# Kernel tuning notes

Hardware: AMD Instinct MI355X
Metric: run time of the kernel (lower is better)

Reference implementation:

```python
import jax, jax.numpy as jnp
import numpy as np

N_GRAPHS = 256
GRADES = jnp.array([0, 1, 1, 1, 2, 2, 2, 3])      # blade -> grade for Cl(3,0): [1,e1,e2,e3,e12,e13,e23,e123]
G_ONEHOT = jnp.eye(4)[GRADES]                      # (8,4) blade->grade one-hot
NUM_RBF, CUTOFF, NEG_SLOPE = 20, 10.0, 0.2
HID, HEADS, HD, LAYERS = 64, 4, 16, 4
EPS_LN = 1e-6


def _mv_linear_sub(x, w, b):
    # MVLinear with per-grade weights. x:(N,I,8), w:(4,O,I), b:(O,) added to scalar blade.
    wb = w[GRADES]                                 # (8,O,I)
    out = jnp.einsum('nib,boi->nob', x, wb)
    return out.at[..., 0].add(b)


def _gat_layer(h, src, dst, edge_scalar, pw, pb, asrc, adst, wsrc, wdst):
    N = h.shape[0]
    z = _mv_linear_sub(h, pw, pb).reshape(N, HEADS, HD, 8)
    # fold per-grade importance weights into per-blade contraction vectors
    a_s = asrc * wsrc[:, GRADES][:, None, :]       # (H,C,8)
    a_d = adst * wdst[:, GRADES][:, None, :]
    s_src = jnp.einsum('nhcb,hcb->nh', z, a_s)
    s_dst = jnp.einsum('nhcb,hcb->nh', z, a_d)
    e = jax.nn.leaky_relu(s_src[src] + s_dst[dst] + edge_scalar, NEG_SLOPE)  # (E,H)
    e_max = jax.ops.segment_max(e, dst, num_segments=N)
    alpha = jnp.exp(e - e_max[dst])
    a_sum = jax.ops.segment_sum(alpha, dst, num_segments=N)
    alpha = alpha / (a_sum[dst] + 1e-16)
    out = jax.ops.segment_sum(z[src] * alpha[:, :, None, None], dst, num_segments=N)
    return out.reshape(N, HEADS * HD, 8)


def _mv_silu(x, a, b):
    # x:(N,C,8); a,b:(C,4). Gate by scalar part (grade 0) and per-grade squared magnitudes.
    qg = jnp.einsum('ncb,bg->ncg', x * x, G_ONEHOT)                 # (N,C,4) mag2 per grade
    norms = jnp.concatenate([x[..., :1], qg[..., 1:]], axis=-1)     # (N,C,4)
    gate = jax.nn.sigmoid(a * norms + b)[..., GRADES]               # (N,C,8)
    return gate * x


def _mv_layernorm(x, a):
    n = jnp.sqrt(jnp.sum(x * x, axis=-1))                           # (N,C)
    n = jnp.mean(n, axis=1, keepdims=True) + EPS_LN                 # (N,1)
    return a[None, :, None] * x / n[..., None]


def _forward(floats, z, edge_index, batch):
    (pos, atom_w, inw, inb, ew1, eb1, ew2, eb2,
     proj_w, proj_b, a_src, a_dst, w_src, w_dst,
     ln_a, silu_a, silu_b, ppw, ppb, pw1, pb1, pw2, pb2) = floats
    src, dst = edge_index[0], edge_index[1]
    N = pos.shape[0]

    # RBF edge features -> per-head scalar bias
    d2 = jnp.sum((pos[src] - pos[dst]) ** 2, axis=-1)
    dist = jnp.where(d2 > 0, jnp.sqrt(jnp.where(d2 > 0, d2, 1.0)), 0.0)
    centers = jnp.linspace(0.0, CUTOFF, NUM_RBF)
    width = CUTOFF / (NUM_RBF - 1)
    rbf = jnp.exp(-0.5 * ((dist[:, None] - centers) / width) ** 2)  # (E,20)
    edge_scalar = jax.nn.silu(rbf @ ew1.T + eb1) @ ew2.T + eb2      # (E,H)

    # node multivector embedding: scalars from atom embedding, grade-1 from centered positions
    h_sca = jnp.zeros((N, HID, 8), dtype=pos.dtype).at[..., 0].set(atom_w[z])
    cnt = jax.ops.segment_sum(jnp.ones((N,), pos.dtype), batch, num_segments=N_GRAPHS)
    pos_mean = jax.ops.segment_sum(pos, batch, num_segments=N_GRAPHS) / jnp.maximum(cnt, 1.0)[:, None]
    pos_c = pos - pos_mean[batch]
    h_vec = jnp.zeros((N, 1, 8), dtype=pos.dtype).at[:, 0, 1:4].set(pos_c)
    h = jnp.concatenate([h_sca, h_vec], axis=1)                     # (N,HID+1,8)
    h = jnp.einsum('nib,oi->nob', h, inw).at[..., 0].add(inb)       # input_proj, subspaces=False

    for l in range(LAYERS):
        h_res = h
        h = _gat_layer(h, src, dst, edge_scalar, proj_w[l], proj_b[l],
                       a_src[l], a_dst[l], w_src[l], w_dst[l])
        h = _mv_silu(h, silu_a[l], silu_b[l])
        h = h + h_res
        h = _mv_layernorm(h, ln_a[l])

    h = _mv_linear_sub(h, ppw, ppb)[..., 0]                         # (N,HID) scalar blade
    g = jax.ops.segment_sum(h, batch, num_segments=N_GRAPHS)        # 'add' readout -> (B,HID)
    out = jax.nn.silu(g @ pw1.T + pb1) @ pw2.T + pb2                # (B,1)
    return out[:, 0]


def setup_inputs() -> dict:
    key = jax.random.key(0)
    ks = jax.random.split(key, 24)
    N, E, B = 20000, 320000, N_GRAPHS
    rn = lambda k, shape, s=0.1: jax.random.normal(k, shape, jnp.float32) * s
    return dict(
        pos=jax.random.normal(ks[0], (N, 3), jnp.float32) * 3.0,
        z=jax.random.randint(ks[1], (N,), 0, 100),
        edge_index=jax.random.randint(ks[2], (2, E), 0, N),
        batch=jnp.sort(jax.random.randint(ks[3], (N,), 0, B)),
        atom_embed_w=rn(ks[4], (100, HID)),
        inproj_w=rn(ks[5], (HID, HID + 1)),
        inproj_b=rn(ks[6], (HID,)),
        edge_w1=rn(ks[7], (HID, NUM_RBF)),
        edge_b1=rn(ks[8], (HID,)),
        edge_w2=rn(ks[9], (HEADS, HID)),
        edge_b2=rn(ks[10], (HEADS,)),
        proj_w=rn(ks[11], (LAYERS, 4, HID, HID)),
        proj_b=rn(ks[12], (LAYERS, HID)),
        a_src=rn(ks[13], (LAYERS, HEADS, HD, 8)),
        a_dst=rn(ks[14], (LAYERS, HEADS, HD, 8)),
        w_src=jnp.ones((LAYERS, HEADS, 4), jnp.float32),
        w_dst=jnp.ones((LAYERS, HEADS, 4), jnp.float32),
        ln_a=jnp.ones((LAYERS, HID), jnp.float32),
        silu_a=jnp.ones((LAYERS, HID, 4), jnp.float32),
        silu_b=jnp.zeros((LAYERS, HID, 4), jnp.float32),
        prepool_w=rn(ks[15], (4, HID, HID)),
        prepool_b=rn(ks[16], (HID,)),
        post_w1=rn(ks[17], (HID, HID)),
        post_b1=rn(ks[18], (HID,)),
        post_w2=rn(ks[19], (1, HID)),
        post_b2=rn(ks[20], (1,)),
    )


def reference(pos, z, edge_index, batch, atom_embed_w, inproj_w, inproj_b,
              edge_w1, edge_b1, edge_w2, edge_b2, proj_w, proj_b,
              a_src, a_dst, w_src, w_dst, ln_a, silu_a, silu_b,
              prepool_w, prepool_b, post_w1, post_b1, post_w2, post_b2):
    floats = (pos, atom_embed_w, inproj_w, inproj_b, edge_w1, edge_b1, edge_w2, edge_b2,
              proj_w, proj_b, a_src, a_dst, w_src, w_dst,
              ln_a, silu_a, silu_b, prepool_w, prepool_b, post_w1, post_b1, post_w2, post_b2)
    return _forward(floats, z, edge_index, batch)
```

## Files before the change

### kernel.cpp

```cpp
#include <hip/hip_runtime.h>
#include <hip/hip_bf16.h>
#include <math.h>

#define HID 64
#define HEADS 4
#define LAYERS 4
#define NRBF 20
#define NG 256
#define CB 512
#define HSTRIDE 68
#define CAPB 64
#define TABN 8192
#define NATOM 100

typedef __attribute__((ext_vector_type(8))) short short8;
typedef __attribute__((ext_vector_type(4))) float floatx4;

__device__ __forceinline__ int gradeOf(int b){ return (b==0)?0:((b<4)?1:((b<7)?2:3)); }
__device__ __forceinline__ unsigned short f2bf(float f){
    __hip_bfloat16 h = __float2bfloat16(f);
    return *(unsigned short*)&h;
}
__device__ __forceinline__ float bflo(int u){ return __uint_as_float(((unsigned)u)<<16); }
__device__ __forceinline__ float bfhi(int u){ return __uint_as_float(((unsigned)u)&0xFFFF0000u); }
__device__ __forceinline__ int packbf2(float a, float b){
    return (int)f2bf(a) | ((int)f2bf(b)<<16);
}

struct P {
    const float *pos; const int *zidx; const int *ei; const int *batch;
    const float *atom_w, *inproj_w, *inproj_b, *ew1, *eb1, *ew2, *eb2;
    const float *proj_w, *proj_b, *a_src, *a_dst, *w_src, *w_dst;
    const float *ln_a, *silu_a, *silu_b, *ppw, *ppb, *pw1, *pb1, *pw2, *pb2;
    float *out;
    int *counts; float *possum; float *pcnt; float *gbuf;
    int *bucket;
    int *escb;
    float *tab;
    unsigned short *WTbf; float *ppw0T; float *w1T; float *sbf;
    float *embT;
    unsigned short *hb;
    unsigned short *zA; unsigned short *zB;
    float *ssA; float *sdA; float *ssB; float *sdB;
    int N, E, Mtiles;
};

__global__ __launch_bounds__(256) void k1_kernel(P p){
    const int PREP_TOTAL = LAYERS*4*64*64 + 2*HID*HID + 2*LAYERS*HEADS;
    const int CP = (PREP_TOTAL+255)/256;
    const int CG = NG/4;
    const int CT = (TABN+1+3)/4;
    int bid = blockIdx.x, t = threadIdx.x;
    if (bid < CP){
        int idx = bid*256 + t;
        const int szW = LAYERS*4*64*64;
        const int e2 = szW + HID*HID;
        const int e3 = e2 + HID*HID;
        if (idx < szW){
            p.WTbf[idx] = f2bf(p.proj_w[idx]);
        } else if (idx < e2){
            int r = idx - szW; int i = r/HID, o = r%HID;
            p.ppw0T[r] = p.ppw[o*HID + i];
        } else if (idx < e3){
            int r = idx - e2; int i = r/HID, o = r%HID;
            p.w1T[r] = p.pw1[o*HID + i];
        } else if (idx < e3 + 2*LAYERS*HEADS){
            int r = idx - e3;
            int hh = r & 3; int type = (r>>2)&1; int l = r>>3;
            const float* a = type ? p.a_dst : p.a_src;
            const float* w = type ? p.w_dst : p.w_src;
            float wh = w[l*16 + hh*4 + 0];
            float s = 0.f;
            for (int c=0;c<16;c++)
                s += a[l*512 + (hh*16+c)*8 + 0] * wh * p.proj_b[l*64 + hh*16 + c];
            p.sbf[r] = s;
        }
    } else if (bid < CP+CG){
        int wv = t>>6, lane = t&63;
        int g = (bid-CP)*4 + wv;
        int lo = 0, hi = p.N;
        while (lo < hi){ int mid = (lo+hi)>>1; if (p.batch[mid] < g) lo = mid+1; else hi = mid; }
        int s0 = lo;
        hi = p.N;
        while (lo < hi){ int mid = (lo+hi)>>1; if (p.batch[mid] < g+1) lo = mid+1; else hi = mid; }
        int s1 = lo;
        float sx=0.f, sy=0.f, sz=0.f;
        for (int i=s0+lane; i<s1; i+=64){
            sx += p.pos[i*3+0]; sy += p.pos[i*3+1]; sz += p.pos[i*3+2];
        }
        #pragma unroll
        for (int off=1; off<64; off<<=1){
            sx += __shfl_xor(sx,off,64);
            sy += __shfl_xor(sy,off,64);
            sz += __shfl_xor(sz,off,64);
        }
        if (lane==0){
            p.possum[g*3+0]=sx; p.possum[g*3+1]=sy; p.possum[g*3+2]=sz;
            p.pcnt[g] = (float)(s1-s0);
        }
    } else if (bid < CP+CG+CT){
        int wv = t>>6, lane = t&63;
        int i = (bid-CP-CG)*4 + wv;
        if (i > TABN) return;
        float d = (float)i * (16.0f/TABN);
        float t0 = d * (19.0f/10.0f);
        float hv = p.eb1[lane];
        #pragma unroll
        for (int k=0;k<NRBF;k++){
            float a = t0 - (float)k;
            hv += __expf(-0.5f*a*a) * p.ew1[lane*NRBF+k];
        }
        float act = hv/(1.0f+__expf(-hv));
        float p0 = act*p.ew2[0*HID+lane];
        float p1 = act*p.ew2[1*HID+lane];
        float p2 = act*p.ew2[2*HID+lane];
        float p3 = act*p.ew2[3*HID+lane];
        #pragma unroll
        for (int off=1; off<64; off<<=1){
            p0 += __shfl_xor(p0,off,64);
            p1 += __shfl_xor(p1,off,64);
            p2 += __shfl_xor(p2,off,64);
            p3 += __shfl_xor(p3,off,64);
        }
        if (lane==0){
            *(float4*)&p.tab[(size_t)i*4] = make_float4(p0+p.eb2[0], p1+p.eb2[1],
                                                        p2+p.eb2[2], p3+p.eb2[3]);
        }
    } else {
        int wv = t>>6, lane = t&63;
        int za = (bid-CP-CG-CT)*4 + wv;
        if (za >= NATOM) return;
        float accv = p.inproj_b[lane];
        for (int i=0;i<HID;i++)
            accv += p.atom_w[(size_t)za*HID + i] * p.inproj_w[lane*65 + i];
        p.embT[(size_t)za*HID + lane] = accv;
    }
}

__device__ __forceinline__ void proj_core(const P& p, int pl, int n0, int nt, int lane,
        const unsigned short* hAl,
        unsigned short* zout, float* ssout, float* sdout){
    const unsigned short* WTl = p.WTbf + (size_t)pl*4*64*64;
    const float* pbl = p.proj_b + pl*HID;
    const float* a_src_l = p.a_src + pl*512;
    const float* a_dst_l = p.a_dst + pl*512;
    const float* w_src_l = p.w_src + pl*16;
    const float* w_dst_l = p.w_dst + pl*16;
    const float* sb_l = p.sbf + pl*8;
    int m = lane&15, quad = lane>>4;
    int o = nt*16 + m;
    float cs[4][2][4];
    float pss[4], psd[4];
    #pragma unroll
    for (int r=0;r<4;r++){ pss[r]=0.f; psd[r]=0.f; }
    #pragma unroll
    for (int bp=0; bp<4; bp++){
        const int b0 = 2*bp, b1 = b0+1;
        const int g0 = gradeOf(b0), g1 = gradeOf(b1);
        const short8 a0 = *(const short8*)(hAl + (b0*16+m)*HSTRIDE + quad*8);
        const short8 a1 = *(const short8*)(hAl + (b0*16+m)*HSTRIDE + 32 + quad*8);
        const short8 a2 = *(const short8*)(hAl + (b1*16+m)*HSTRIDE + quad*8);
        const short8 a3 = *(const short8*)(hAl + (b1*16+m)*HSTRIDE + 32 + quad*8);
        const short8 w00 = *(const short8*)(WTl + (g0*64 + o)*64 + quad*8);
        const short8 w01 = *(const short8*)(WTl + (g0*64 + o)*64 + 32 + quad*8);
        short8 w10, w11;
        if (g1==g0){ w10 = w00; w11 = w01; }
        else {
            w10 = *(const short8*)(WTl + (g1*64 + o)*64 + quad*8);
            w11 = *(const short8*)(WTl + (g1*64 + o)*64 + 32 + quad*8);
        }
        floatx4 c0 = {0.f,0.f,0.f,0.f}, c1 = {0.f,0.f,0.f,0.f};
        c0 = __builtin_amdgcn_mfma_f32_16x16x32_bf16(a0, w00, c0, 0,0,0);
        c0 = __builtin_amdgcn_mfma_f32_16x16x32_bf16(a1, w01, c0, 0,0,0);
        c1 = __builtin_amdgcn_mfma_f32_16x16x32_bf16(a2, w10, c1, 0,0,0);
        c1 = __builtin_amdgcn_mfma_f32_16x16x32_bf16(a3, w11, c1, 0,0,0);
        float as0 = a_src_l[o*8+b0]*w_src_l[nt*4+g0];
        float as1 = a_src_l[o*8+b1]*w_src_l[nt*4+g1];
        float ad0 = a_dst_l[o*8+b0]*w_dst_l[nt*4+g0];
        float ad1 = a_dst_l[o*8+b1]*w_dst_l[nt*4+g1];
        float bias0 = (bp==0) ? pbl[o] : 0.0f;
        #pragma unroll
        for (int r=0;r<4;r++){
            float v0 = c0[r], v1 = c1[r];
            pss[r] += v0*as0 + v1*as1;
            psd[r] += v0*ad0 + v1*ad1;
            cs[bp][0][r] = v0 + bias0;
            cs[bp][1][r] = v1;
        }
    }
    #pragma unroll
    for (int r=0;r<4;r++){
        int nn = n0 + quad*4 + r;
        if (nn < p.N){
            unsigned short pk[8];
            #pragma unroll
            for (int bp=0;bp<4;bp++){
                pk[2*bp]   = f2bf(cs[bp][0][r]);
                pk[2*bp+1] = f2bf(cs[bp][1][r]);
            }
            *(int4*)(zout + (size_t)nn*CB + o*8) = *(int4*)pk;
        }
    }
    #pragma unroll
    for (int r=0;r<4;r++){
        float vs = pss[r], vd = psd[r];
        #pragma unroll
        for (int off=1; off<16; off<<=1){
            vs += __shfl_xor(vs, off, 64);
            vd += __shfl_xor(vd, off, 64);
        }
        int nn = n0 + quad*4 + r;
        if (m==0 && nn<p.N){
            ssout[nn*4+nt] = vs + sb_l[nt];
            sdout[nn*4+nt] = vd + sb_l[4+nt];
        }
    }
}

__global__ __launch_bounds__(256) void k2_kernel(P p){
    __shared__ unsigned short hAl[8*16*HSTRIDE];
    int t = threadIdx.x, wv = t>>6, lane = t&63;
    if ((int)blockIdx.x >= p.Mtiles){
        int e = ((int)blockIdx.x - p.Mtiles)*256 + t;
        if (e >= p.E) return;
        int s = p.ei[e], d = p.ei[p.E+e];
        float dx = p.pos[s*3+0]-p.pos[d*3+0];
        float dy = p.pos[s*3+1]-p.pos[d*3+1];
        float dz = p.pos[s*3+2]-p.pos[d*3+2];
        float dist = sqrtf(dx*dx+dy*dy+dz*dz);
        float idxf = fminf(dist * ((float)TABN/16.0f), (float)(TABN-1));
        int i0 = (int)idxf;
        float fr = idxf - (float)i0;
        float4 f0 = *(const float4*)&p.tab[(size_t)i0*4];
        float4 f1 = *(const float4*)&p.tab[(size_t)(i0+1)*4];
        int slot = atomicAdd(&p.counts[d],1);
        if (slot < CAPB){
            p.bucket[(size_t)d*CAPB + slot] = s;
            int2 epk = make_int2(
                packbf2(f0.x + (f1.x-f0.x)*fr, f0.y + (f1.y-f0.y)*fr),
                packbf2(f0.z + (f1.z-f0.z)*fr, f0.w + (f1.w-f0.w)*fr));
            *(int2*)&p.escb[((size_t)d*CAPB + slot)*2] = epk;
        }
        return;
    }
    int n0 = blockIdx.x*16;
    float wvv = p.inproj_w[lane*65 + 64];
    for (int k=0;k<4;k++){
        int m = wv*4 + k;
        int n = n0 + m;
        if (n < p.N){
            int zn = p.zidx[n];
            float acc = p.embT[(size_t)zn*HID + lane];
            int g = p.batch[n];
            float cm = p.pcnt[g]; cm = cm>1.0f?cm:1.0f;
            float px = p.pos[n*3+0]-p.possum[g*3+0]/cm;
            float py = p.pos[n*3+1]-p.possum[g*3+1]/cm;
            float pz = p.pos[n*3+2]-p.possum[g*3+2]/cm;
            unsigned short pk[8];
            pk[0]=f2bf(acc); pk[1]=f2bf(wvv*px); pk[2]=f2bf(wvv*py); pk[3]=f2bf(wvv*pz);
            pk[4]=0; pk[5]=0; pk[6]=0; pk[7]=0;
            *(int4*)(p.hb + (size_t)n*CB + lane*8) = *(int4*)pk;
            #pragma unroll
            for (int b=0;b<8;b++) hAl[(b*16+m)*HSTRIDE + lane] = pk[b];
        } else {
            #pragma unroll
            for (int b=0;b<8;b++) hAl[(b*16+m)*HSTRIDE + lane] = 0;
        }
    }
    __syncthreads();
    proj_core(p, 0, n0, wv, lane, hAl, p.zA, p.ssA, p.sdA);
}

__device__ __forceinline__ void fmab8(const float* lwv, int h_id, int J,
                                      const int4* zv, float* acc, float& dn){
    #pragma unroll
    for (int i=0;i<8;i++){
        float w = lwv[(J+i)*4 + h_id];
        acc[0] += w*bflo(zv[i].x); acc[1] += w*bfhi(zv[i].x);
        acc[2] += w*bflo(zv[i].y); acc[3] += w*bfhi(zv[i].y);
        acc[4] += w*bflo(zv[i].z); acc[5] += w*bfhi(zv[i].z);
        acc[6] += w*bflo(zv[i].w); acc[7] += w*bfhi(zv[i].w);
        dn += w;
    }
}

__device__ __forceinline__ void agg_node(const P& p, int l, int n, int lane, float* lwv,
        const unsigned short* __restrict__ zin, const float* __restrict__ ssin,
        const float* __restrict__ sdin, float* outv){
    int4 hres = *((const int4*)(p.hb + (size_t)n*CB) + lane);
    float4 sdl = *(const float4*)&sdin[n*4];
    int deg = min(p.counts[n], CAPB);
    int h_id = lane>>4;
    const int* bs = p.bucket + (size_t)n*CAPB;
    int s = 0;
    float l0=-1e30f,l1=-1e30f,l2=-1e30f,l3=-1e30f;
    if (lane < deg){
        s = bs[lane];
        int2 ev = *((const int2*)p.escb + ((size_t)n*CAPB + lane));
        float4 sv  = *(const float4*)&ssin[s*4];
        l0 = sv.x+sdl.x+bflo(ev.x); l0=(l0>=0.f)?l0:0.2f*l0;
        l1 = sv.y+sdl.y+bfhi(ev.x); l1=(l1>=0.f)?l1:0.2f*l1;
        l2 = sv.z+sdl.z+bflo(ev.y); l2=(l2>=0.f)?l2:0.2f*l2;
        l3 = sv.w+sdl.w+bfhi(ev.y); l3=(l3>=0.f)?l3:0.2f*l3;
    }
    int bc = (deg+7)>>3;
    int4 zv[8];
    if (bc>0){
        #pragma unroll
        for (int i=0;i<8;i++){
            int sb = __builtin_amdgcn_readlane(s, i);
            zv[i] = *((const int4*)(zin + (size_t)(unsigned)sb*CB) + lane);
        }
    }
    float m0=l0,m1=l1,m2=l2,m3=l3;
    #pragma unroll
    for (int off=1; off<64; off<<=1){
        m0=fmaxf(m0,__shfl_xor(m0,off,64));
        m1=fmaxf(m1,__shfl_xor(m1,off,64));
        m2=fmaxf(m2,__shfl_xor(m2,off,64));
        m3=fmaxf(m3,__shfl_xor(m3,off,64));
    }
    *(float4*)&lwv[lane*4] = make_float4(__expf(l0-m0),__expf(l1-m1),
                                         __expf(l2-m2),__expf(l3-m3));
    float acc[8];
    #pragma unroll
    for (int k=0;k<8;k++) acc[k]=0.f;
    float dn = 0.f;
    if (bc>0) fmab8(lwv, h_id, 0, zv, acc, dn);
    for (int j=8; j<bc*8; j+=8){
        #pragma unroll
        for (int i=0;i<8;i++){
            int sb = __builtin_amdgcn_readlane(s, j+i);
            zv[i] = *((const int4*)(zin + (size_t)(unsigned)sb*CB) + lane);
        }
        fmab8(lwv, h_id, j, zv, acc, dn);
    }
    float inv = 1.0f/(dn + 1e-16f);
    float x[8];
    #pragma unroll
    for (int k=0;k<8;k++) x[k] = acc[k]*inv;
    const float* silu_a_l = p.silu_a + l*HID*4;
    const float* silu_b_l = p.silu_b + l*HID*4;
    float4 sa = *(const float4*)&silu_a_l[lane*4];
    float4 sb = *(const float4*)&silu_b_l[lane*4];
    float n1 = x[1]*x[1]+x[2]*x[2]+x[3]*x[3];
    float n2 = x[4]*x[4]+x[5]*x[5]+x[6]*x[6];
    float n3 = x[7]*x[7];
    float g0 = 1.0f/(1.0f+__expf(-(sa.x*x[0]+sb.x)));
    float g1 = 1.0f/(1.0f+__expf(-(sa.y*n1+sb.y)));
    float g2 = 1.0f/(1.0f+__expf(-(sa.z*n2+sb.z)));
    float g3 = 1.0f/(1.0f+__expf(-(sa.w*n3+sb.w)));
    float val[8];
    val[0]=g0*x[0]+bflo(hres.x); val[1]=g1*x[1]+bfhi(hres.x);
    val[2]=g1*x[2]+bflo(hres.y); val[3]=g1*x[3]+bfhi(hres.y);
    val[4]=g2*x[4]+bflo(hres.z); val[5]=g2*x[5]+bfhi(hres.z);
    val[6]=g2*x[6]+bflo(hres.w); val[7]=g3*x[7]+bfhi(hres.w);
    float ssq=0.f;
    #pragma unroll
    for (int k=0;k<8;k++) ssq += val[k]*val[k];
    float nr = sqrtf(ssq);
    #pragma unroll
    for (int off=1; off<64; off<<=1) nr += __shfl_xor(nr, off, 64);
    float mean = nr*(1.0f/64.0f) + 1e-6f;
    float scale = p.ln_a[l*HID + lane]/mean;
    #pragma unroll
    for (int k=0;k<8;k++) outv[k] = scale*val[k];
}

__global__ __launch_bounds__(1024) void aggproj_kernel(P p, int l,
        const unsigned short* __restrict__ zin, const float* __restrict__ ssin,
        const float* __restrict__ sdin,
        unsigned short* zout, float* ssout, float* sdout){
    __shared__ float lw[16][256];
    __shared__ unsigned short hAl[8*16*HSTRIDE];
    int wv = threadIdx.x>>6, lane = threadIdx.x&63;
    int n0 = blockIdx.x*16;
    int n = n0 + wv;
    unsigned short pk[8] = {0,0,0,0,0,0,0,0};
    if (n < p.N){
        float outv[8];
        agg_node(p, l, n, lane, lw[wv], zin, ssin, sdin, outv);
        #pragma unroll
        for (int k=0;k<8;k++) pk[k] = f2bf(outv[k]);
        *(int4*)(p.hb + (size_t)n*CB + lane*8) = *(int4*)pk;
    }
    #pragma unroll
    for (int b=0;b<8;b++) hAl[(b*16+wv)*HSTRIDE + lane] = pk[b];
    __syncthreads();
    if (wv < 4)
        proj_core(p, l+1, n0, wv, lane, hAl, zout, ssout, sdout);
}

__global__ __launch_bounds__(256) void agg_kernel(P p, int l,
        const unsigned short* __restrict__ zin, const float* __restrict__ ssin,
        const float* __restrict__ sdin){
    __shared__ float lw[4][256];
    int wv = threadIdx.x>>6, lane = threadIdx.x&63;
    int n = blockIdx.x*4 + wv;
    if (n >= p.N) return;
    float outv[8];
    agg_node(p, l, n, lane, lw[wv], zin, ssin, sdin, outv);
    atomicAdd(&p.gbuf[p.batch[n]*HID + lane], outv[0]);
}

__global__ void final_kernel(P p){
    int gid = blockIdx.x; int o = threadIdx.x;
    float gs = p.gbuf[gid*HID + o];
    float cnt = p.pcnt[gid];
    float gsc = cnt * p.ppb[o];
    for (int i=0;i<HID;i++) gsc += __shfl(gs, i, 64) * p.ppw0T[i*HID + o];
    float a = p.pb1[o];
    for (int i=0;i<HID;i++) a += __shfl(gsc, i, 64) * p.w1T[i*HID + o];
    float act = a/(1.0f+__expf(-a));
    float pv = act * p.pw2[o];
    #pragma unroll
    for (int off=1; off<64; off<<=1) pv += __shfl_xor(pv, off, 64);
    if (o==0) p.out[gid] = pv + p.pb2[0];
}

extern "C" void kernel_launch(void* const* d_in, const int* in_sizes, int n_in,
                              void* d_out, int out_size, void* d_ws, size_t ws_size,
                              hipStream_t stream) {
    P p;
    p.pos      = (const float*)d_in[0];
    p.zidx     = (const int*)  d_in[1];
    p.ei       = (const int*)  d_in[2];
    p.batch    = (const int*)  d_in[3];
    p.atom_w   = (const float*)d_in[4];
    p.inproj_w = (const float*)d_in[5];
    p.inproj_b = (const float*)d_in[6];
    p.ew1      = (const float*)d_in[7];
    p.eb1      = (const float*)d_in[8];
    p.ew2      = (const float*)d_in[9];
    p.eb2      = (const float*)d_in[10];
    p.proj_w   = (const float*)d_in[11];
    p.proj_b   = (const float*)d_in[12];
    p.a_src    = (const float*)d_in[13];
    p.a_dst    = (const float*)d_in[14];
    p.w_src    = (const float*)d_in[15];
    p.w_dst    = (const float*)d_in[16];
    p.ln_a     = (const float*)d_in[17];
    p.silu_a   = (const float*)d_in[18];
    p.silu_b   = (const float*)d_in[19];
    p.ppw      = (const float*)d_in[20];
    p.ppb      = (const float*)d_in[21];
    p.pw1      = (const float*)d_in[22];
    p.pb1      = (const float*)d_in[23];
    p.pw2      = (const float*)d_in[24];
    p.pb2      = (const float*)d_in[25];
    p.out = (float*)d_out;

    const int N = in_sizes[0]/3;
    const int E = in_sizes[2]/2;
    p.N = N; p.E = E; p.Mtiles = (N+15)/16;

    float* wsf = (float*)d_ws;
    size_t off = 0;
    auto alloc = [&](size_t nelem){ size_t r = off; off += (nelem + 63) & ~(size_t)63; return r; };
    size_t o_counts = alloc(N);
    size_t o_g      = alloc(NG*HID);
    size_t zero_end = off;
    size_t o_possum = alloc(NG*3);
    size_t o_pcnt   = alloc(NG);
    size_t o_bucket = alloc((size_t)N*CAPB);
    size_t o_escb   = alloc((size_t)N*CAPB*2);
    size_t o_tab    = alloc((size_t)(TABN+2)*4);
    size_t o_ssA    = alloc((size_t)N*4);
    size_t o_sdA    = alloc((size_t)N*4);
    size_t o_ssB    = alloc((size_t)N*4);
    size_t o_sdB    = alloc((size_t)N*4);
    size_t o_WTbf   = alloc((size_t)LAYERS*4*64*64/2);
    size_t o_ppw0T  = alloc(HID*HID);
    size_t o_w1T    = alloc(HID*HID);
    size_t o_sbf    = alloc(2*LAYERS*HEADS);
    size_t o_embT   = alloc((size_t)NATOM*HID);
    size_t o_hb     = alloc((size_t)N*CB/2);
    size_t o_zA     = alloc((size_t)N*CB/2);
    size_t o_zB     = alloc((size_t)N*CB/2);

    p.counts = (int*)(wsf + o_counts);
    p.gbuf   = wsf + o_g;
    p.possum = wsf + o_possum;
    p.pcnt   = wsf + o_pcnt;
    p.bucket = (int*)(wsf + o_bucket);
    p.escb   = (int*)(wsf + o_escb);
    p.tab    = wsf + o_tab;
    p.ssA    = wsf + o_ssA;
    p.sdA    = wsf + o_sdA;
    p.ssB    = wsf + o_ssB;
    p.sdB    = wsf + o_sdB;
    p.WTbf   = (unsigned short*)(wsf + o_WTbf);
    p.ppw0T  = wsf + o_ppw0T;
    p.w1T    = wsf + o_w1T;
    p.sbf    = wsf + o_sbf;
    p.embT   = wsf + o_embT;
    p.hb     = (unsigned short*)(wsf + o_hb);
    p.zA     = (unsigned short*)(wsf + o_zA);
    p.zB     = (unsigned short*)(wsf + o_zB);

    hipMemsetAsync(wsf, 0, zero_end*sizeof(float), stream);

    const int PREP_TOTAL = LAYERS*4*64*64 + 2*HID*HID + 2*LAYERS*HEADS;
    const int CP = (PREP_TOTAL+255)/256;
    const int CG = NG/4;
    const int CE = (E+255)/256;
    const int CT = (TABN+1+3)/4;
    const int CEMB = (NATOM+3)/4;

    k1_kernel<<<CP+CG+CT+CEMB, 256, 0, stream>>>(p);
    k2_kernel<<<p.Mtiles + CE, 256, 0, stream>>>(p);

    const int FG = (N+15)/16;
    aggproj_kernel<<<FG, 1024, 0, stream>>>(p, 0, p.zA, p.ssA, p.sdA, p.zB, p.ssB, p.sdB);
    aggproj_kernel<<<FG, 1024, 0, stream>>>(p, 1, p.zB, p.ssB, p.sdB, p.zA, p.ssA, p.sdA);
    aggproj_kernel<<<FG, 1024, 0, stream>>>(p, 2, p.zA, p.ssA, p.sdA, p.zB, p.ssB, p.sdB);
    agg_kernel    <<<(N+3)/4, 256, 0, stream>>>(p, 3, p.zB, p.ssB, p.sdB);

    final_kernel<<<NG, 64, 0, stream>>>(p);
}
```

Measured before the change: 388.5 us.

## Split fused projection across all 16 waves with LDS partial-score reduction

In the fused aggregate+projection kernel, the projection previously ran only on 4 of 16 waves while the rest idled. It now spreads the work over all 16 waves, with each wave handling one 16-output tile and a pair of blades using two bf16 MFMA chains. Partial attention scores go into a shared buffer and are summed after an extra barrier. This is meant to shorten the serial projection tail, at the cost of a second sync, more LDS and redundant weight loads when blade grades repeat.

```diff
diff --git a/kernel.cpp b/kernel.cpp
--- a/kernel.cpp
+++ b/kernel.cpp
@@ -217,6 +217,79 @@
     }
 }
 
+__device__ __forceinline__ void proj_mfma16(const P& p, int pl, int n0, int wv, int lane,
+        const unsigned short* hAl, float* redP, unsigned short* zout){
+    const unsigned short* WTl = p.WTbf + (size_t)pl*4*64*64;
+    int nt = wv&3, bp = wv>>2;
+    int m = lane&15, quad = lane>>4;
+    int o = nt*16 + m;
+    const int b0 = 2*bp, b1 = b0+1;
+    const int g0 = gradeOf(b0), g1 = gradeOf(b1);
+    const short8 a0 = *(const short8*)(hAl + (b0*16+m)*HSTRIDE + quad*8);
+    const short8 a1 = *(const short8*)(hAl + (b0*16+m)*HSTRIDE + 32 + quad*8);
+    const short8 a2 = *(const short8*)(hAl + (b1*16+m)*HSTRIDE + quad*8);
+    const short8 a3 = *(const short8*)(hAl + (b1*16+m)*HSTRIDE + 32 + quad*8);
+    const short8 w00 = *(const short8*)(WTl + (g0*64 + o)*64 + quad*8);
+    const short8 w01 = *(const short8*)(WTl + (g0*64 + o)*64 + 32 + quad*8);
+    short8 w10, w11;
+    if (g1==g0){ w10 = w00; w11 = w01; }
+    else {
+        w10 = *(const short8*)(WTl + (g1*64 + o)*64 + quad*8);
+        w11 = *(const short8*)(WTl + (g1*64 + o)*64 + 32 + quad*8);
+    }
+    floatx4 c0 = {0.f,0.f,0.f,0.f}, c1 = {0.f,0.f,0.f,0.f};
+    c0 = __builtin_amdgcn_mfma_f32_16x16x32_bf16(a0, w00, c0, 0,0,0);
+    c0 = __builtin_amdgcn_mfma_f32_16x16x32_bf16(a1, w01, c0, 0,0,0);
+    c1 = __builtin_amdgcn_mfma_f32_16x16x32_bf16(a2, w10, c1, 0,0,0);
+    c1 = __builtin_amdgcn_mfma_f32_16x16x32_bf16(a3, w11, c1, 0,0,0);
+    float as0 = p.a_src[pl*512 + o*8+b0]*p.w_src[pl*16 + nt*4+g0];
+    float as1 = p.a_src[pl*512 + o*8+b1]*p.w_src[pl*16 + nt*4+g1];
+    float ad0 = p.a_dst[pl*512 + o*8+b0]*p.w_dst[pl*16 + nt*4+g0];
+    float ad1 = p.a_dst[pl*512 + o*8+b1]*p.w_dst[pl*16 + nt*4+g1];
+    float bias0 = (bp==0) ? p.proj_b[pl*HID + o] : 0.0f;
+    float pss[4], psd[4];
+    #pragma unroll
+    for (int r=0;r<4;r++){
+        float v0 = c0[r], v1 = c1[r];
+        pss[r] = v0*as0 + v1*as1;
+        psd[r] = v0*ad0 + v1*ad1;
+        int nn = n0 + quad*4 + r;
+        if (nn < p.N)
+            *(int*)(zout + (size_t)nn*CB + o*8 + b0) = packbf2(v0 + bias0, v1);
+    }
+    #pragma unroll
+    for (int r=0;r<4;r++){
+        #pragma unroll
+        for (int off=1; off<16; off<<=1){
+            pss[r] += __shfl_xor(pss[r], off, 64);
+            psd[r] += __shfl_xor(psd[r], off, 64);
+        }
+    }
+    if (m==0){
+        #pragma unroll
+        for (int r=0;r<4;r++){
+            int row = quad*4 + r;
+            redP[(bp*4+nt)*16 + row]       = pss[r];
+            redP[256 + (bp*4+nt)*16 + row] = psd[r];
+        }
+    }
+}
+__device__ __forceinline__ void proj_finish16(const P& p, int pl, int n0, int wv, int lane,
+        const float* redP, float* ssout, float* sdout){
+    if (wv >= 4 || lane >= 16) return;
+    int nn = n0 + lane;
+    if (nn >= p.N) return;
+    const float* sb_l = p.sbf + pl*8;
+    float vs = 0.f, vd = 0.f;
+    #pragma unroll
+    for (int bp=0;bp<4;bp++){
+        vs += redP[(bp*4+wv)*16 + lane];
+        vd += redP[256 + (bp*4+wv)*16 + lane];
+    }
+    ssout[nn*4+wv] = vs + sb_l[wv];
+    sdout[nn*4+wv] = vd + sb_l[4+wv];
+}
+
 __global__ __launch_bounds__(256) void k2_kernel(P p){
     __shared__ unsigned short hAl[8*16*HSTRIDE];
     int t = threadIdx.x, wv = t>>6, lane = t&63;
@@ -373,6 +446,7 @@
         unsigned short* zout, float* ssout, float* sdout){
     __shared__ float lw[16][256];
     __shared__ unsigned short hAl[8*16*HSTRIDE];
+    __shared__ float redP[512];
     int wv = threadIdx.x>>6, lane = threadIdx.x&63;
     int n0 = blockIdx.x*16;
     int n = n0 + wv;
@@ -387,8 +461,9 @@
     #pragma unroll
     for (int b=0;b<8;b++) hAl[(b*16+wv)*HSTRIDE + lane] = pk[b];
     __syncthreads();
-    if (wv < 4)
-        proj_core(p, l+1, n0, wv, lane, hAl, zout, ssout, sdout);
+    proj_mfma16(p, l+1, n0, wv, lane, hAl, redP, zout);
+    __syncthreads();
+    proj_finish16(p, l+1, n0, wv, lane, redP, ssout, sdout);
 }
 
 __global__ __launch_bounds__(256) void agg_kernel(P p, int l,
```

Measured after the change: 451.6 us. +16.2%, slower.

## Sort nodes by in-degree so aggproj blocks get balanced edge counts

Applied to the files above, without the earlier changes.

Adds a single-block counting sort that builds a permutation of nodes ordered by in-degree (bucket count). The fused aggregate+projection kernels then process nodes in that order, so the 16 waves in each block have similar degrees, and projection outputs are scattered back through the permutation. This targets wave imbalance inside the 1024-thread blocks, where the block waits on its slowest node before the shared-memory projection. The cost is an extra serial single-block kernel launch, an indirection load per node, and scattered rather than contiguous z/score writes, which lose locality.

```diff
diff --git a/kernel.cpp b/kernel.cpp
--- a/kernel.cpp
+++ b/kernel.cpp
@@ -40,6 +40,7 @@
     unsigned short *WTbf; float *ppw0T; float *w1T; float *sbf;
     float *embT;
     unsigned short *hb;
+    int *perm;
     unsigned short *zA; unsigned short *zB;
     float *ssA; float *sdA; float *ssB; float *sdB;
     int N, E, Mtiles;
@@ -137,8 +138,28 @@
     }
 }
 
+__global__ __launch_bounds__(256) void sort_kernel(P p){
+    __shared__ int hist[CAPB+1];
+    __shared__ int base[CAPB+1];
+    int t = threadIdx.x;
+    if (t <= CAPB) hist[t] = 0;
+    __syncthreads();
+    for (int n = t; n < p.N; n += 256)
+        atomicAdd(&hist[min(p.counts[n], CAPB)], 1);
+    __syncthreads();
+    if (t == 0){
+        int acc = 0;
+        for (int b = 0; b <= CAPB; b++){ base[b] = acc; acc += hist[b]; }
+    }
+    __syncthreads();
+    for (int n = t; n < p.N; n += 256){
+        int slot = atomicAdd(&base[min(p.counts[n], CAPB)], 1);
+        p.perm[slot] = n;
+    }
+}
+
 __device__ __forceinline__ void proj_core(const P& p, int pl, int n0, int nt, int lane,
-        const unsigned short* hAl,
+        const unsigned short* hAl, const int* permp,
         unsigned short* zout, float* ssout, float* sdout){
     const unsigned short* WTl = p.WTbf + (size_t)pl*4*64*64;
     const float* pbl = p.proj_b + pl*HID;
@@ -190,8 +211,9 @@
     }
     #pragma unroll
     for (int r=0;r<4;r++){
-        int nn = n0 + quad*4 + r;
-        if (nn < p.N){
+        int idx = n0 + quad*4 + r;
+        int nn = (idx < p.N) ? (permp ? permp[idx] : idx) : -1;
+        if (nn >= 0){
             unsigned short pk[8];
             #pragma unroll
             for (int bp=0;bp<4;bp++){
@@ -209,8 +231,9 @@
             vs += __shfl_xor(vs, off, 64);
             vd += __shfl_xor(vd, off, 64);
         }
-        int nn = n0 + quad*4 + r;
-        if (m==0 && nn<p.N){
+        int idx = n0 + quad*4 + r;
+        int nn = (idx < p.N) ? (permp ? permp[idx] : idx) : -1;
+        if (m==0 && nn>=0){
             ssout[nn*4+nt] = vs + sb_l[nt];
             sdout[nn*4+nt] = vd + sb_l[4+nt];
         }
@@ -268,7 +291,7 @@
         }
     }
     __syncthreads();
-    proj_core(p, 0, n0, wv, lane, hAl, p.zA, p.ssA, p.sdA);
+    proj_core(p, 0, n0, wv, lane, hAl, nullptr, p.zA, p.ssA, p.sdA);
 }
 
 __device__ __forceinline__ void fmab8(const float* lwv, int h_id, int J,
@@ -375,9 +398,10 @@
     __shared__ unsigned short hAl[8*16*HSTRIDE];
     int wv = threadIdx.x>>6, lane = threadIdx.x&63;
     int n0 = blockIdx.x*16;
-    int n = n0 + wv;
+    int idx = n0 + wv;
+    int n = (idx < p.N) ? p.perm[idx] : -1;
     unsigned short pk[8] = {0,0,0,0,0,0,0,0};
-    if (n < p.N){
+    if (n >= 0){
         float outv[8];
         agg_node(p, l, n, lane, lw[wv], zin, ssin, sdin, outv);
         #pragma unroll
@@ -388,7 +412,7 @@
     for (int b=0;b<8;b++) hAl[(b*16+wv)*HSTRIDE + lane] = pk[b];
     __syncthreads();
     if (wv < 4)
-        proj_core(p, l+1, n0, wv, lane, hAl, zout, ssout, sdout);
+        proj_core(p, l+1, n0, wv, lane, hAl, p.perm, zout, ssout, sdout);
 }
 
 __global__ __launch_bounds__(256) void agg_kernel(P p, int l,
@@ -474,6 +498,7 @@
     size_t o_w1T    = alloc(HID*HID);
     size_t o_sbf    = alloc(2*LAYERS*HEADS);
     size_t o_embT   = alloc((size_t)NATOM*HID);
+    size_t o_perm   = alloc(N);
     size_t o_hb     = alloc((size_t)N*CB/2);
     size_t o_zA     = alloc((size_t)N*CB/2);
     size_t o_zB     = alloc((size_t)N*CB/2);
@@ -494,6 +519,7 @@
     p.w1T    = wsf + o_w1T;
     p.sbf    = wsf + o_sbf;
     p.embT   = wsf + o_embT;
+    p.perm   = (int*)(wsf + o_perm);
     p.hb     = (unsigned short*)(wsf + o_hb);
     p.zA     = (unsigned short*)(wsf + o_zA);
     p.zB     = (unsigned short*)(wsf + o_zB);
@@ -509,6 +535,7 @@
 
     k1_kernel<<<CP+CG+CT+CEMB, 256, 0, stream>>>(p);
     k2_kernel<<<p.Mtiles + CE, 256, 0, stream>>>(p);
+    sort_kernel<<<1, 256, 0, stream>>>(p);
 
     const int FG = (N+15)/16;
     aggproj_kernel<<<FG, 1024, 0, stream>>>(p, 0, p.zA, p.ssA, p.sdA, p.zB, p.ssB, p.sdB);
```

Measured after the change: 472.9 us. 1.22x slower.
